# Kernel tuning notes

Measured on AMD Instinct MI355X. Metric: run time of the kernel, lower is better.

Reference implementation:

```python
import jax, jax.numpy as jnp
import numpy as np

N_CLUSTERS = 512
TEMPERATURE = 0.1


def setup_inputs() -> dict:
    key = jax.random.key(0)
    k1, k2 = jax.random.split(key)
    x = jax.random.normal(k1, (32, 1024, 256), dtype=jnp.float32)
    centroids = jax.random.normal(k2, (N_CLUSTERS, 256), dtype=jnp.float32)
    return {"x": x, "centroids": centroids}


def reference(x, centroids):
    # Flatten non-cluster axes into a sample axis: [N, D]
    B, S, D = x.shape
    xf = x.reshape(-1, D)  # [N, D]
    x_sq = jnp.sum(xf * xf, axis=-1, keepdims=True)           # [N, 1]
    c_sq = jnp.sum(centroids * centroids, axis=-1)             # [K]
    cross = jnp.einsum('nd,kd->nk', xf, centroids)             # [N, K]
    dists = x_sq - 2.0 * cross + c_sq[None, :]                 # [N, K]
    # Temperature-scaled soft assignments
    assignments = jax.nn.softmax(-dists / TEMPERATURE, axis=-1)  # [N, K]
    # Restore leading (non-feature) dims, append cluster axis
    return assignments.reshape(B, S, N_CLUSTERS)
```

## Files before the change

### kernel.cpp

```cpp
#include <hip/hip_runtime.h>

#define NROWS 32768
#define KC 512
#define DDIM 256
#define BM 128
#define BK 32
#define KCH (DDIM / BK)
#define CHUNK_USH (KC * BK)

typedef __attribute__((ext_vector_type(8))) short bf16x8;
typedef __attribute__((ext_vector_type(4))) float f32x4;

union U8 { unsigned short u[8]; bf16x8 v; };

__device__ __forceinline__ unsigned short f2bf(float f) {
    union { float f; unsigned int u; } a; a.f = f;
    unsigned int r = a.u + 0x7fffu + ((a.u >> 16) & 1u);
    return (unsigned short)(r >> 16);
}
__device__ __forceinline__ float bf2f(unsigned short h) {
    union { unsigned int u; float f; } a; a.u = ((unsigned int)h) << 16;
    return a.f;
}
__device__ __forceinline__ void ld16(const void* g, void* l) {
    __builtin_amdgcn_global_load_lds(
        (const __attribute__((address_space(1))) unsigned int*)g,
        (__attribute__((address_space(3))) unsigned int*)l, 16, 0, 0);
}

__global__ __launch_bounds__(64) void prep_c(const float* __restrict__ c,
                                             unsigned short* __restrict__ bhi,
                                             unsigned short* __restrict__ blo,
                                             float* __restrict__ csq10) {
    const int n = blockIdx.x, lane = threadIdx.x;
    const int d0 = lane * 4;
    float4 v = ((const float4*)(c + (size_t)n * DDIM))[lane];
    float vv[4] = {v.x, v.y, v.z, v.w};
    unsigned short hh[4], ll[4];
    float ssq = 0.f;
    #pragma unroll
    for (int i = 0; i < 4; ++i) {
        ssq += vv[i] * vv[i];
        hh[i] = f2bf(vv[i]);
        ll[i] = f2bf(vv[i] - bf2f(hh[i]));
    }
    #pragma unroll
    for (int off = 32; off; off >>= 1) ssq += __shfl_xor(ssq, off);
    if (lane == 0) csq10[n] = 10.f * ssq;
    const int ks = d0 >> 5;
    const int q  = (d0 >> 3) & 3;
    const int s  = q ^ ((n >> 1) & 3);
    const size_t dst = (size_t)ks * CHUNK_USH + (n * 4 + s) * 8 + (d0 & 7);
    *(ushort4*)(bhi + dst) = make_ushort4(hh[0], hh[1], hh[2], hh[3]);
    *(ushort4*)(blo + dst) = make_ushort4(ll[0], ll[1], ll[2], ll[3]);
}

union SmemU {
    struct { unsigned short Bh[2][CHUNK_USH], Bl[2][CHUNK_USH]; } k;
    float lbuf[32 * 516];
};

__global__ __launch_bounds__(512, 2) void kmeans_mfma(
    const float* __restrict__ x, const unsigned short* __restrict__ bhi,
    const unsigned short* __restrict__ blo, const float* __restrict__ csq10,
    float* __restrict__ out) {
    __shared__ __align__(16) SmemU sm;
    __shared__ float red[2][2][BM];

    const int tid  = threadIdx.x;
    const int w    = tid >> 6, lane = tid & 63;
    const int wm   = w >> 1, wn = w & 1;
    const int cc   = lane & 15, q = lane >> 4;
    const int row0 = blockIdx.x * BM;

    f32x4 acc[2][16];
    #pragma unroll
    for (int mt = 0; mt < 2; ++mt)
        #pragma unroll
        for (int t = 0; t < 16; ++t) acc[mt][t] = (f32x4){0.f, 0.f, 0.f, 0.f};

    const float* xA0 = x + (size_t)(row0 + wm * 32 + cc) * DDIM + q * 8;
    const float* xA1 = xA0 + (size_t)16 * DDIM;
    const int sF = q ^ ((cc >> 1) & 3);
    const int bF = (4 * cc + sF) * 8;
    const int dmaOff = (w * 4) * 512;

    float4 c00 = *(const float4*)xA0;
    float4 c01 = *(const float4*)(xA0 + 4);
    float4 c10 = *(const float4*)xA1;
    float4 c11 = *(const float4*)(xA1 + 4);
    #pragma unroll
    for (int j = 0; j < 4; ++j) {
        const int o = dmaOff + j * 512;
        ld16(bhi + o + lane * 8, &sm.k.Bh[0][o]);
        ld16(blo + o + lane * 8, &sm.k.Bl[0][o]);
    }

    #pragma unroll
    for (int ks = 0; ks < KCH; ++ks) {
        const int pp = ks & 1;
        bf16x8 ah[2], al[2];
        {
            float v0[8] = {c00.x, c00.y, c00.z, c00.w, c01.x, c01.y, c01.z, c01.w};
            float v1[8] = {c10.x, c10.y, c10.z, c10.w, c11.x, c11.y, c11.z, c11.w};
            U8 H0, L0, H1, L1;
            #pragma unroll
            for (int e = 0; e < 8; ++e) {
                H0.u[e] = f2bf(v0[e]); L0.u[e] = f2bf(v0[e] - bf2f(H0.u[e]));
                H1.u[e] = f2bf(v1[e]); L1.u[e] = f2bf(v1[e] - bf2f(H1.u[e]));
            }
            ah[0] = H0.v; al[0] = L0.v; ah[1] = H1.v; al[1] = L1.v;
        }
        float4 n00, n01, n10, n11;
        if (ks < KCH - 1) {
            const int kn = (ks + 1) * BK;
            n00 = *(const float4*)(xA0 + kn);
            n01 = *(const float4*)(xA0 + kn + 4);
            n10 = *(const float4*)(xA1 + kn);
            n11 = *(const float4*)(xA1 + kn + 4);
        }
        __builtin_amdgcn_sched_barrier(0);
        if (ks < KCH - 1) {
            asm volatile("s_waitcnt vmcnt(4)" ::: "memory");
        } else {
            asm volatile("s_waitcnt vmcnt(0)" ::: "memory");
        }
        __builtin_amdgcn_s_barrier();
        __builtin_amdgcn_sched_barrier(0);
        if (ks < KCH - 1) {
            const size_t cb = (size_t)(ks + 1) * CHUNK_USH;
            #pragma unroll
            for (int j = 0; j < 4; ++j) {
                const int o = dmaOff + j * 512;
                ld16(bhi + cb + o + lane * 8, &sm.k.Bh[1 - pp][o]);
                ld16(blo + cb + o + lane * 8, &sm.k.Bl[1 - pp][o]);
            }
        }
        #pragma unroll
        for (int t = 0; t < 16; ++t) {
            const int bo = (wn * 16 + t) * 512 + bF;
            bf16x8 bh = *(const bf16x8*)&sm.k.Bh[pp][bo];
            bf16x8 bl = *(const bf16x8*)&sm.k.Bl[pp][bo];
            acc[0][t] = __builtin_amdgcn_mfma_f32_16x16x32_bf16(ah[0], bh, acc[0][t], 0, 0, 0);
            acc[1][t] = __builtin_amdgcn_mfma_f32_16x16x32_bf16(ah[1], bh, acc[1][t], 0, 0, 0);
            acc[0][t] = __builtin_amdgcn_mfma_f32_16x16x32_bf16(ah[0], bl, acc[0][t], 0, 0, 0);
            acc[1][t] = __builtin_amdgcn_mfma_f32_16x16x32_bf16(ah[1], bl, acc[1][t], 0, 0, 0);
            acc[0][t] = __builtin_amdgcn_mfma_f32_16x16x32_bf16(al[0], bh, acc[0][t], 0, 0, 0);
            acc[1][t] = __builtin_amdgcn_mfma_f32_16x16x32_bf16(al[1], bh, acc[1][t], 0, 0, 0);
        }
        c00 = n00; c01 = n01; c10 = n10; c11 = n11;
    }

    float csqv[16];
    #pragma unroll
    for (int t = 0; t < 16; ++t) csqv[t] = csq10[wn * 256 + t * 16 + cc];
    const int rb = wm * 32 + q * 4;
    float M[2][4], I[2][4];
    #pragma unroll
    for (int mt = 0; mt < 2; ++mt)
        #pragma unroll
        for (int g = 0; g < 4; ++g) {
            float pm = -1e30f;
            #pragma unroll
            for (int t = 0; t < 16; ++t) pm = fmaxf(pm, 20.f * acc[mt][t][g] - csqv[t]);
            #pragma unroll
            for (int off = 1; off < 16; off <<= 1) pm = fmaxf(pm, __shfl_xor(pm, off));
            if (cc == 0) red[0][wn][rb + mt * 16 + g] = pm;
            M[mt][g] = pm;
        }
    __syncthreads();
    #pragma unroll
    for (int mt = 0; mt < 2; ++mt)
        #pragma unroll
        for (int g = 0; g < 4; ++g) {
            M[mt][g] = fmaxf(M[mt][g], red[0][1 - wn][rb + mt * 16 + g]);
            float ps = 0.f;
            #pragma unroll
            for (int t = 0; t < 16; ++t) ps += __expf(20.f * acc[mt][t][g] - csqv[t] - M[mt][g]);
            #pragma unroll
            for (int off = 1; off < 16; off <<= 1) ps += __shfl_xor(ps, off);
            if (cc == 0) red[1][wn][rb + mt * 16 + g] = ps;
        }
    __syncthreads();
    #pragma unroll
    for (int mt = 0; mt < 2; ++mt)
        #pragma unroll
        for (int g = 0; g < 4; ++g)
            I[mt][g] = 1.f / (red[1][0][rb + mt * 16 + g] + red[1][1][rb + mt * 16 + g]);

    #pragma unroll
    for (int p = 0; p < 4; ++p) {
        if (wm == p) {
            #pragma unroll
            for (int mt = 0; mt < 2; ++mt)
                #pragma unroll
                for (int g = 0; g < 4; ++g) {
                    const int   lr = mt * 16 + q * 4 + g;
                    const float mg = M[mt][g], ig = I[mt][g];
                    #pragma unroll
                    for (int t = 0; t < 16; ++t)
                        sm.lbuf[lr * 516 + wn * 256 + t * 16 + cc] =
                            __expf(20.f * acc[mt][t][g] - csqv[t] - mg) * ig;
                }
        }
        __syncthreads();
        #pragma unroll
        for (int j = 0; j < 8; ++j) {
            const int f    = j * 512 + tid;
            const int lrow = f >> 7;
            const int c4   = f & 127;
            float4    v    = *(const float4*)&sm.lbuf[lrow * 516 + c4 * 4];
            *(float4*)(out + (size_t)(row0 + p * 32 + lrow) * KC + c4 * 4) = v;
        }
        __syncthreads();
    }
}

extern "C" void kernel_launch(void* const* d_in, const int* in_sizes, int n_in,
                              void* d_out, int out_size, void* d_ws, size_t ws_size,
                              hipStream_t stream) {
    const float* x   = (const float*)d_in[0];
    const float* c   = (const float*)d_in[1];
    float*       out = (float*)d_out;

    unsigned short* bhi   = (unsigned short*)d_ws;
    unsigned short* blo   = bhi + (size_t)KCH * CHUNK_USH;
    float*          csq10 = (float*)(blo + (size_t)KCH * CHUNK_USH);

    prep_c<<<KC, 64, 0, stream>>>(c, bhi, blo, csq10);
    kmeans_mfma<<<NROWS / BM, 512, 0, stream>>>(x, bhi, blo, csq10, out);
}
```

Measured before the change: 117.6 us.

## Split MFMA loop into phases with interleaved DMA, setprio, direct output stores

Each K-chunk's 16 MFMA tiles are split into four phases. Each phase loads its B fragments from LDS, issues one slice of the next chunk's global-to-LDS copy, and runs its MFMAs under raised wave priority, with barriers between phases. The epilogue drops the LDS staging buffer and its four-pass synchronised copy-out, and writes softmax results directly to global memory with 4-byte strided stores. This cuts LDS use and epilogue barriers, but adds extra barriers in the main loop, and the output writes are less coalesced (16 consecutive floats per row group instead of full float4 rows).

New measurement: 123.0 us. +4.6%, slower.

```diff
diff --git a/kernel.cpp b/kernel.cpp
--- a/kernel.cpp
+++ b/kernel.cpp
@@ -55,16 +55,13 @@
     *(ushort4*)(blo + dst) = make_ushort4(ll[0], ll[1], ll[2], ll[3]);
 }
 
-union SmemU {
-    struct { unsigned short Bh[2][CHUNK_USH], Bl[2][CHUNK_USH]; } k;
-    float lbuf[32 * 516];
-};
+struct SmemK { unsigned short Bh[2][CHUNK_USH], Bl[2][CHUNK_USH]; };
 
 __global__ __launch_bounds__(512, 2) void kmeans_mfma(
     const float* __restrict__ x, const unsigned short* __restrict__ bhi,
     const unsigned short* __restrict__ blo, const float* __restrict__ csq10,
     float* __restrict__ out) {
-    __shared__ __align__(16) SmemU sm;
+    __shared__ __align__(16) SmemK sm;
     __shared__ float red[2][2][BM];
 
     const int tid  = threadIdx.x;
@@ -92,8 +89,8 @@
     #pragma unroll
     for (int j = 0; j < 4; ++j) {
         const int o = dmaOff + j * 512;
-        ld16(bhi + o + lane * 8, &sm.k.Bh[0][o]);
-        ld16(blo + o + lane * 8, &sm.k.Bl[0][o]);
+        ld16(bhi + o + lane * 8, &sm.Bh[0][o]);
+        ld16(blo + o + lane * 8, &sm.Bl[0][o]);
     }
 
     #pragma unroll
@@ -127,26 +124,39 @@
         }
         __builtin_amdgcn_s_barrier();
         __builtin_amdgcn_sched_barrier(0);
-        if (ks < KCH - 1) {
-            const size_t cb = (size_t)(ks + 1) * CHUNK_USH;
-            #pragma unroll
-            for (int j = 0; j < 4; ++j) {
-                const int o = dmaOff + j * 512;
-                ld16(bhi + cb + o + lane * 8, &sm.k.Bh[1 - pp][o]);
-                ld16(blo + cb + o + lane * 8, &sm.k.Bl[1 - pp][o]);
-            }
-        }
-        #pragma unroll
-        for (int t = 0; t < 16; ++t) {
-            const int bo = (wn * 16 + t) * 512 + bF;
-            bf16x8 bh = *(const bf16x8*)&sm.k.Bh[pp][bo];
-            bf16x8 bl = *(const bf16x8*)&sm.k.Bl[pp][bo];
-            acc[0][t] = __builtin_amdgcn_mfma_f32_16x16x32_bf16(ah[0], bh, acc[0][t], 0, 0, 0);
-            acc[1][t] = __builtin_amdgcn_mfma_f32_16x16x32_bf16(ah[1], bh, acc[1][t], 0, 0, 0);
-            acc[0][t] = __builtin_amdgcn_mfma_f32_16x16x32_bf16(ah[0], bl, acc[0][t], 0, 0, 0);
-            acc[1][t] = __builtin_amdgcn_mfma_f32_16x16x32_bf16(ah[1], bl, acc[1][t], 0, 0, 0);
-            acc[0][t] = __builtin_amdgcn_mfma_f32_16x16x32_bf16(al[0], bh, acc[0][t], 0, 0, 0);
-            acc[1][t] = __builtin_amdgcn_mfma_f32_16x16x32_bf16(al[1], bh, acc[1][t], 0, 0, 0);
+
+        #pragma unroll
+        for (int ph = 0; ph < 4; ++ph) {
+            bf16x8 bh[4], bl[4];
+            #pragma unroll
+            for (int tt = 0; tt < 4; ++tt) {
+                const int bo = (wn * 16 + ph * 4 + tt) * 512 + bF;
+                bh[tt] = *(const bf16x8*)&sm.Bh[pp][bo];
+                bl[tt] = *(const bf16x8*)&sm.Bl[pp][bo];
+            }
+            if (ks < KCH - 1) {
+                const size_t cb = (size_t)(ks + 1) * CHUNK_USH;
+                const int o = dmaOff + ph * 512;
+                ld16(bhi + cb + o + lane * 8, &sm.Bh[1 - pp][o]);
+                ld16(blo + cb + o + lane * 8, &sm.Bl[1 - pp][o]);
+            }
+            __builtin_amdgcn_s_barrier();
+            asm volatile("s_waitcnt lgkmcnt(0)" ::: "memory");
+            __builtin_amdgcn_sched_barrier(0);
+            __builtin_amdgcn_s_setprio(1);
+            #pragma unroll
+            for (int tt = 0; tt < 4; ++tt) {
+                const int t = ph * 4 + tt;
+                acc[0][t] = __builtin_amdgcn_mfma_f32_16x16x32_bf16(ah[0], bh[tt], acc[0][t], 0, 0, 0);
+                acc[1][t] = __builtin_amdgcn_mfma_f32_16x16x32_bf16(ah[1], bh[tt], acc[1][t], 0, 0, 0);
+                acc[0][t] = __builtin_amdgcn_mfma_f32_16x16x32_bf16(ah[0], bl[tt], acc[0][t], 0, 0, 0);
+                acc[1][t] = __builtin_amdgcn_mfma_f32_16x16x32_bf16(ah[1], bl[tt], acc[1][t], 0, 0, 0);
+                acc[0][t] = __builtin_amdgcn_mfma_f32_16x16x32_bf16(al[0], bh[tt], acc[0][t], 0, 0, 0);
+                acc[1][t] = __builtin_amdgcn_mfma_f32_16x16x32_bf16(al[1], bh[tt], acc[1][t], 0, 0, 0);
+            }
+            __builtin_amdgcn_s_setprio(0);
+            __builtin_amdgcn_sched_barrier(0);
+            __builtin_amdgcn_s_barrier();
         }
         c00 = n00; c01 = n01; c10 = n10; c11 = n11;
     }
@@ -189,31 +199,16 @@
             I[mt][g] = 1.f / (red[1][0][rb + mt * 16 + g] + red[1][1][rb + mt * 16 + g]);
 
     #pragma unroll
-    for (int p = 0; p < 4; ++p) {
-        if (wm == p) {
-            #pragma unroll
-            for (int mt = 0; mt < 2; ++mt)
-                #pragma unroll
-                for (int g = 0; g < 4; ++g) {
-                    const int   lr = mt * 16 + q * 4 + g;
-                    const float mg = M[mt][g], ig = I[mt][g];
-                    #pragma unroll
-                    for (int t = 0; t < 16; ++t)
-                        sm.lbuf[lr * 516 + wn * 256 + t * 16 + cc] =
-                            __expf(20.f * acc[mt][t][g] - csqv[t] - mg) * ig;
-                }
-        }
-        __syncthreads();
-        #pragma unroll
-        for (int j = 0; j < 8; ++j) {
-            const int f    = j * 512 + tid;
-            const int lrow = f >> 7;
-            const int c4   = f & 127;
-            float4    v    = *(const float4*)&sm.lbuf[lrow * 516 + c4 * 4];
-            *(float4*)(out + (size_t)(row0 + p * 32 + lrow) * KC + c4 * 4) = v;
-        }
-        __syncthreads();
-    }
+    for (int mt = 0; mt < 2; ++mt)
+        #pragma unroll
+        for (int g = 0; g < 4; ++g) {
+            const float mg = M[mt][g], ig = I[mt][g];
+            float* orow = out + (size_t)(row0 + wm * 32 + mt * 16 + q * 4 + g) * KC
+                              + wn * 256 + cc;
+            #pragma unroll
+            for (int t = 0; t < 16; ++t)
+                orow[t * 16] = __expf(20.f * acc[mt][t][g] - csqv[t] - mg) * ig;
+        }
 }
 
 extern "C" void kernel_launch(void* const* d_in, const int* in_sizes, int n_in,
```

## Switch split-bf16 GEMM from 16x16x32 to 32x32x16 MFMA tiles

Applied to the files above, without the earlier changes.

Replaces the 16x16x32 bf16 MFMA tiling with 32x32x16 MFMA instructions. This changes the centroid LDS layout written by the prep kernel, how the A fragments are loaded from x, and the softmax epilogue's row/column mapping. The larger MFMA tile lowers the ratio of LDS fragment reads to MFMA work and issues fewer instructions per FLOP. In exchange, the softmax reductions now need 32-lane shuffles and the LDS reads are no longer swizzled, which may cause bank conflicts.

New measurement: 129.9 us. 1.1x slower.

```diff
diff --git a/kernel.cpp b/kernel.cpp
--- a/kernel.cpp
+++ b/kernel.cpp
@@ -9,7 +9,7 @@
 #define CHUNK_USH (KC * BK)
 
 typedef __attribute__((ext_vector_type(8))) short bf16x8;
-typedef __attribute__((ext_vector_type(4))) float f32x4;
+typedef __attribute__((ext_vector_type(16))) float f32x16;
 
 union U8 { unsigned short u[8]; bf16x8 v; };
 
@@ -47,10 +47,13 @@
     #pragma unroll
     for (int off = 32; off; off >>= 1) ssq += __shfl_xor(ssq, off);
     if (lane == 0) csq10[n] = 10.f * ssq;
-    const int ks = d0 >> 5;
-    const int q  = (d0 >> 3) & 3;
-    const int s  = q ^ ((n >> 1) & 3);
-    const size_t dst = (size_t)ks * CHUNK_USH + (n * 4 + s) * 8 + (d0 & 7);
+    const int ks   = d0 >> 5;
+    const int s    = (d0 >> 4) & 1;
+    const int half = (d0 >> 3) & 1;
+    const int e    = d0 & 7;
+    const int T32  = n >> 5, c32 = n & 31;
+    const size_t dst = (((size_t)ks * 16 + T32) * 2 + s) * 512
+                     + (half * 32 + c32) * 8 + e;
     *(ushort4*)(bhi + dst) = make_ushort4(hh[0], hh[1], hh[2], hh[3]);
     *(ushort4*)(blo + dst) = make_ushort4(ll[0], ll[1], ll[2], ll[3]);
 }
@@ -70,25 +73,22 @@
     const int tid  = threadIdx.x;
     const int w    = tid >> 6, lane = tid & 63;
     const int wm   = w >> 1, wn = w & 1;
-    const int cc   = lane & 15, q = lane >> 4;
+    const int c32  = lane & 31, hi = lane >> 5;
     const int row0 = blockIdx.x * BM;
 
-    f32x4 acc[2][16];
-    #pragma unroll
-    for (int mt = 0; mt < 2; ++mt)
-        #pragma unroll
-        for (int t = 0; t < 16; ++t) acc[mt][t] = (f32x4){0.f, 0.f, 0.f, 0.f};
-
-    const float* xA0 = x + (size_t)(row0 + wm * 32 + cc) * DDIM + q * 8;
-    const float* xA1 = xA0 + (size_t)16 * DDIM;
-    const int sF = q ^ ((cc >> 1) & 3);
-    const int bF = (4 * cc + sF) * 8;
+    f32x16 acc[8];
+    #pragma unroll
+    for (int t = 0; t < 8; ++t)
+        #pragma unroll
+        for (int g = 0; g < 16; ++g) acc[t][g] = 0.f;
+
+    const float* xA = x + (size_t)(row0 + wm * 32 + c32) * DDIM + hi * 8;
     const int dmaOff = (w * 4) * 512;
 
-    float4 c00 = *(const float4*)xA0;
-    float4 c01 = *(const float4*)(xA0 + 4);
-    float4 c10 = *(const float4*)xA1;
-    float4 c11 = *(const float4*)(xA1 + 4);
+    float4 c00 = *(const float4*)xA;
+    float4 c01 = *(const float4*)(xA + 4);
+    float4 c10 = *(const float4*)(xA + 16);
+    float4 c11 = *(const float4*)(xA + 20);
     #pragma unroll
     for (int j = 0; j < 4; ++j) {
         const int o = dmaOff + j * 512;
@@ -114,10 +114,10 @@
         float4 n00, n01, n10, n11;
         if (ks < KCH - 1) {
             const int kn = (ks + 1) * BK;
-            n00 = *(const float4*)(xA0 + kn);
-            n01 = *(const float4*)(xA0 + kn + 4);
-            n10 = *(const float4*)(xA1 + kn);
-            n11 = *(const float4*)(xA1 + kn + 4);
+            n00 = *(const float4*)(xA + kn);
+            n01 = *(const float4*)(xA + kn + 4);
+            n10 = *(const float4*)(xA + kn + 16);
+            n11 = *(const float4*)(xA + kn + 20);
         }
         __builtin_amdgcn_sched_barrier(0);
         if (ks < KCH - 1) {
@@ -137,71 +137,79 @@
             }
         }
         #pragma unroll
-        for (int t = 0; t < 16; ++t) {
-            const int bo = (wn * 16 + t) * 512 + bF;
-            bf16x8 bh = *(const bf16x8*)&sm.k.Bh[pp][bo];
-            bf16x8 bl = *(const bf16x8*)&sm.k.Bl[pp][bo];
-            acc[0][t] = __builtin_amdgcn_mfma_f32_16x16x32_bf16(ah[0], bh, acc[0][t], 0, 0, 0);
-            acc[1][t] = __builtin_amdgcn_mfma_f32_16x16x32_bf16(ah[1], bh, acc[1][t], 0, 0, 0);
-            acc[0][t] = __builtin_amdgcn_mfma_f32_16x16x32_bf16(ah[0], bl, acc[0][t], 0, 0, 0);
-            acc[1][t] = __builtin_amdgcn_mfma_f32_16x16x32_bf16(ah[1], bl, acc[1][t], 0, 0, 0);
-            acc[0][t] = __builtin_amdgcn_mfma_f32_16x16x32_bf16(al[0], bh, acc[0][t], 0, 0, 0);
-            acc[1][t] = __builtin_amdgcn_mfma_f32_16x16x32_bf16(al[1], bh, acc[1][t], 0, 0, 0);
-        }
+        for (int s = 0; s < 2; ++s)
+            #pragma unroll
+            for (int grp = 0; grp < 2; ++grp) {
+                bf16x8 bh[4], bl[4];
+                #pragma unroll
+                for (int j = 0; j < 4; ++j) {
+                    const int bo = ((wn * 8 + grp * 4 + j) * 2 + s) * 512 + lane * 8;
+                    bh[j] = *(const bf16x8*)&sm.k.Bh[pp][bo];
+                    bl[j] = *(const bf16x8*)&sm.k.Bl[pp][bo];
+                }
+                #pragma unroll
+                for (int j = 0; j < 4; ++j)
+                    acc[grp * 4 + j] = __builtin_amdgcn_mfma_f32_32x32x16_bf16(
+                        ah[s], bh[j], acc[grp * 4 + j], 0, 0, 0);
+                #pragma unroll
+                for (int j = 0; j < 4; ++j)
+                    acc[grp * 4 + j] = __builtin_amdgcn_mfma_f32_32x32x16_bf16(
+                        ah[s], bl[j], acc[grp * 4 + j], 0, 0, 0);
+                #pragma unroll
+                for (int j = 0; j < 4; ++j)
+                    acc[grp * 4 + j] = __builtin_amdgcn_mfma_f32_32x32x16_bf16(
+                        al[s], bh[j], acc[grp * 4 + j], 0, 0, 0);
+            }
         c00 = n00; c01 = n01; c10 = n10; c11 = n11;
     }
 
-    float csqv[16];
-    #pragma unroll
-    for (int t = 0; t < 16; ++t) csqv[t] = csq10[wn * 256 + t * 16 + cc];
-    const int rb = wm * 32 + q * 4;
-    float M[2][4], I[2][4];
-    #pragma unroll
-    for (int mt = 0; mt < 2; ++mt)
-        #pragma unroll
-        for (int g = 0; g < 4; ++g) {
-            float pm = -1e30f;
-            #pragma unroll
-            for (int t = 0; t < 16; ++t) pm = fmaxf(pm, 20.f * acc[mt][t][g] - csqv[t]);
-            #pragma unroll
-            for (int off = 1; off < 16; off <<= 1) pm = fmaxf(pm, __shfl_xor(pm, off));
-            if (cc == 0) red[0][wn][rb + mt * 16 + g] = pm;
-            M[mt][g] = pm;
-        }
+    float csqv[8];
+    #pragma unroll
+    for (int t = 0; t < 8; ++t) csqv[t] = csq10[wn * 256 + t * 32 + c32];
+    float M[16], I[16];
+    #pragma unroll
+    for (int g = 0; g < 16; ++g) {
+        const int rg = (g & 3) + 8 * (g >> 2) + 4 * hi;
+        float pm = -1e30f;
+        #pragma unroll
+        for (int t = 0; t < 8; ++t) pm = fmaxf(pm, fmaf(20.f, acc[t][g], -csqv[t]));
+        #pragma unroll
+        for (int off = 1; off < 32; off <<= 1) pm = fmaxf(pm, __shfl_xor(pm, off));
+        if (c32 == 0) red[0][wn][wm * 32 + rg] = pm;
+        M[g] = pm;
+    }
     __syncthreads();
     #pragma unroll
-    for (int mt = 0; mt < 2; ++mt)
-        #pragma unroll
-        for (int g = 0; g < 4; ++g) {
-            M[mt][g] = fmaxf(M[mt][g], red[0][1 - wn][rb + mt * 16 + g]);
-            float ps = 0.f;
-            #pragma unroll
-            for (int t = 0; t < 16; ++t) ps += __expf(20.f * acc[mt][t][g] - csqv[t] - M[mt][g]);
-            #pragma unroll
-            for (int off = 1; off < 16; off <<= 1) ps += __shfl_xor(ps, off);
-            if (cc == 0) red[1][wn][rb + mt * 16 + g] = ps;
-        }
+    for (int g = 0; g < 16; ++g) {
+        const int rg = (g & 3) + 8 * (g >> 2) + 4 * hi;
+        const int ri = wm * 32 + rg;
+        M[g] = fmaxf(M[g], red[0][1 - wn][ri]);
+        float ps = 0.f;
+        #pragma unroll
+        for (int t = 0; t < 8; ++t) ps += __expf(fmaf(20.f, acc[t][g], -csqv[t]) - M[g]);
+        #pragma unroll
+        for (int off = 1; off < 32; off <<= 1) ps += __shfl_xor(ps, off);
+        if (c32 == 0) red[1][wn][ri] = ps;
+    }
     __syncthreads();
     #pragma unroll
-    for (int mt = 0; mt < 2; ++mt)
-        #pragma unroll
-        for (int g = 0; g < 4; ++g)
-            I[mt][g] = 1.f / (red[1][0][rb + mt * 16 + g] + red[1][1][rb + mt * 16 + g]);
+    for (int g = 0; g < 16; ++g) {
+        const int ri = wm * 32 + (g & 3) + 8 * (g >> 2) + 4 * hi;
+        I[g] = 1.f / (red[1][0][ri] + red[1][1][ri]);
+    }
 
     #pragma unroll
     for (int p = 0; p < 4; ++p) {
         if (wm == p) {
             #pragma unroll
-            for (int mt = 0; mt < 2; ++mt)
-                #pragma unroll
-                for (int g = 0; g < 4; ++g) {
-                    const int   lr = mt * 16 + q * 4 + g;
-                    const float mg = M[mt][g], ig = I[mt][g];
-                    #pragma unroll
-                    for (int t = 0; t < 16; ++t)
-                        sm.lbuf[lr * 516 + wn * 256 + t * 16 + cc] =
-                            __expf(20.f * acc[mt][t][g] - csqv[t] - mg) * ig;
-                }
+            for (int g = 0; g < 16; ++g) {
+                const int   lr = (g & 3) + 8 * (g >> 2) + 4 * hi;
+                const float mg = M[g], ig = I[g];
+                #pragma unroll
+                for (int t = 0; t < 8; ++t)
+                    sm.lbuf[lr * 516 + wn * 256 + t * 32 + c32] =
+                        __expf(fmaf(20.f, acc[t][g], -csqv[t]) - mg) * ig;
+            }
         }
         __syncthreads();
         #pragma unroll
```
